# Kernel tuning notes

Measured on AMD Instinct MI355X. Metric: run time of the kernel, lower is better.

Reference implementation:

```python
import jax, jax.numpy as jnp
import numpy as np

N_NODES = 50000
N_EDGES = 1250000
D_FEAT = 64


def setup_inputs() -> dict:
    key = jax.random.key(0)
    k1, k2, k3, k4 = jax.random.split(key, 4)
    feat = jax.random.normal(k1, (N_NODES, D_FEAT), dtype=jnp.float32)
    edge_weight = jax.random.uniform(k2, (N_EDGES,), dtype=jnp.float32)
    edge_src = jax.random.randint(k3, (N_EDGES,), 0, N_NODES, dtype=jnp.int64)
    edge_dst = jnp.sort(jax.random.randint(k4, (N_EDGES,), 0, N_NODES, dtype=jnp.int64))
    return {"feat": feat, "edge_weight": edge_weight,
            "edge_src": edge_src, "edge_dst": edge_dst}


def reference(feat, edge_weight, edge_src, edge_dst):
    # u_mul_e: gather source node features, scale by per-edge weight
    msgs = feat[edge_src] * edge_weight[:, None]          # [E, d]
    # fn.sum: scatter-add messages to destination nodes
    rst = jax.ops.segment_sum(msgs, edge_dst, num_segments=N_NODES)  # [N, d]
    return rst
```

## Files before the change

kernel.cpp:

```cpp
#include <hip/hip_runtime.h>
#include <hip/hip_fp16.h>

#define D_FEAT 64

__global__ __launch_bounds__(256) void build_rowptr_scatter(
    const int* __restrict__ edge_dst, int* __restrict__ rp,
    int n_edges, int n_nodes) {
  const int e = blockIdx.x * blockDim.x + threadIdx.x;
  if (e > n_edges) return;
  const int d0 = (e == 0) ? -1 : edge_dst[e - 1];
  const int d1 = (e == n_edges) ? n_nodes : edge_dst[e];
  for (int v = d0 + 1; v <= d1; ++v) rp[v] = e;
}

__global__ __launch_bounds__(256) void repack_f16(
    const float* __restrict__ feat, uint2* __restrict__ f16,
    int n_vec4) {
  const int i = blockIdx.x * blockDim.x + threadIdx.x;
  if (i >= n_vec4) return;
  const float4 v = ((const float4*)feat)[i];
  const __half2 h0 = __float22half2_rn(make_float2(v.x, v.y));
  const __half2 h1 = __float22half2_rn(make_float2(v.z, v.w));
  uint2 o;
  o.x = *(const unsigned int*)&h0;
  o.y = *(const unsigned int*)&h1;
  f16[i] = o;
}

__global__ __launch_bounds__(256) void gcn_gather_f16(
    const uint4* __restrict__ feat16,
    const float* __restrict__ ew,
    const int* __restrict__ esrc,
    const int* __restrict__ rp,
    float* __restrict__ out, int n_nodes) {
  const int wave = (blockIdx.x * blockDim.x + threadIdx.x) >> 6;
  const int lane = threadIdx.x & 63;
  if (wave >= n_nodes) return;
  const int slot = lane >> 3;
  const int part = lane & 7;

  const int e0 = rp[wave];
  const int e1 = rp[wave + 1];

  float a0 = 0.f, a1 = 0.f, a2 = 0.f, a3 = 0.f;
  float a4 = 0.f, a5 = 0.f, a6 = 0.f, a7 = 0.f;

  for (int base = e0; base < e1; base += 64) {
    const int n = min(64, e1 - base);
    int   s = 0;
    float w = 0.0f;
    if (lane < n) {
      s = esrc[base + lane];
      w = ew[base + lane];
    }
#pragma unroll
    for (int r = 0; r < 8; ++r) {
      const int   sk = __shfl(s, r * 8 + slot);
      const float wk = __shfl(w, r * 8 + slot);
      const uint4 q  = feat16[(size_t)sk * 8 + part];
      const float2 f0 = __half22float2(*(const __half2*)&q.x);
      const float2 f1 = __half22float2(*(const __half2*)&q.y);
      const float2 f2 = __half22float2(*(const __half2*)&q.z);
      const float2 f3 = __half22float2(*(const __half2*)&q.w);
      a0 = fmaf(f0.x, wk, a0); a1 = fmaf(f0.y, wk, a1);
      a2 = fmaf(f1.x, wk, a2); a3 = fmaf(f1.y, wk, a3);
      a4 = fmaf(f2.x, wk, a4); a5 = fmaf(f2.y, wk, a5);
      a6 = fmaf(f3.x, wk, a6); a7 = fmaf(f3.y, wk, a7);
    }
  }

#pragma unroll
  for (int m = 8; m <= 32; m <<= 1) {
    a0 += __shfl_xor(a0, m); a1 += __shfl_xor(a1, m);
    a2 += __shfl_xor(a2, m); a3 += __shfl_xor(a3, m);
    a4 += __shfl_xor(a4, m); a5 += __shfl_xor(a5, m);
    a6 += __shfl_xor(a6, m); a7 += __shfl_xor(a7, m);
  }

  if (slot == 0) {
    float4* orow = (float4*)(out + (size_t)wave * D_FEAT);
    orow[part * 2]     = make_float4(a0, a1, a2, a3);
    orow[part * 2 + 1] = make_float4(a4, a5, a6, a7);
  }
}

extern "C" void kernel_launch(void* const* d_in, const int* in_sizes, int n_in,
                              void* d_out, int out_size, void* d_ws, size_t ws_size,
                              hipStream_t stream) {
  const float* feat        = (const float*)d_in[0];
  const float* edge_weight = (const float*)d_in[1];
  const int*   edge_src    = (const int*)d_in[2];
  const int*   edge_dst    = (const int*)d_in[3];
  float* out = (float*)d_out;

  const int n_edges = in_sizes[1];
  const int n_nodes = out_size / D_FEAT;

  int*  rp     = (int*)d_ws;
  uint2* f16   = (uint2*)((char*)d_ws + (1 << 20));

  const int bp_threads = n_edges + 1;
  build_rowptr_scatter<<<(bp_threads + 255) / 256, 256, 0, stream>>>(
      edge_dst, rp, n_edges, n_nodes);

  const int n_vec4 = n_nodes * (D_FEAT / 4);
  repack_f16<<<(n_vec4 + 255) / 256, 256, 0, stream>>>(feat, f16, n_vec4);

  const long total_threads = (long)n_nodes * 64;
  gcn_gather_f16<<<(int)((total_threads + 255) / 256), 256, 0, stream>>>(
      (const uint4*)f16, edge_weight, edge_src, rp, out, n_nodes);
}
```

Baseline: 105.7 us.

## Merge prep kernels into one launch and warm per-XCD caches in gather

The row-pointer build and the f16 feature repack now run in a single launch, with blocks split by index, which removes one kernel launch and its dependency gap. The gather kernel also starts with a prologue where the first blocks on each XCD (blockIdx>>3) read the whole f16 feature table, so it is resident in that XCD's L2 before the random gathers begin. The warm-up adds about 6.4 MB of reads per XCD at kernel start and assumes round-robin block-to-XCD placement.

Result: slower. 110.5 us (+4.5%).

```diff
diff --git a/kernel.cpp b/kernel.cpp
--- a/kernel.cpp
+++ b/kernel.cpp
@@ -3,28 +3,27 @@
 
 #define D_FEAT 64
 
-__global__ __launch_bounds__(256) void build_rowptr_scatter(
+__global__ __launch_bounds__(256) void prep_kernel(
+    const float* __restrict__ feat, uint2* __restrict__ f16,
     const int* __restrict__ edge_dst, int* __restrict__ rp,
-    int n_edges, int n_nodes) {
-  const int e = blockIdx.x * blockDim.x + threadIdx.x;
-  if (e > n_edges) return;
-  const int d0 = (e == 0) ? -1 : edge_dst[e - 1];
-  const int d1 = (e == n_edges) ? n_nodes : edge_dst[e];
-  for (int v = d0 + 1; v <= d1; ++v) rp[v] = e;
-}
-
-__global__ __launch_bounds__(256) void repack_f16(
-    const float* __restrict__ feat, uint2* __restrict__ f16,
-    int n_vec4) {
-  const int i = blockIdx.x * blockDim.x + threadIdx.x;
-  if (i >= n_vec4) return;
-  const float4 v = ((const float4*)feat)[i];
-  const __half2 h0 = __float22half2_rn(make_float2(v.x, v.y));
-  const __half2 h1 = __float22half2_rn(make_float2(v.z, v.w));
-  uint2 o;
-  o.x = *(const unsigned int*)&h0;
-  o.y = *(const unsigned int*)&h1;
-  f16[i] = o;
+    int n_vec4, int n_edges, int n_nodes, int rb) {
+  if ((int)blockIdx.x < rb) {
+    const int i = blockIdx.x * blockDim.x + threadIdx.x;
+    if (i >= n_vec4) return;
+    const float4 v = ((const float4*)feat)[i];
+    const __half2 h0 = __float22half2_rn(make_float2(v.x, v.y));
+    const __half2 h1 = __float22half2_rn(make_float2(v.z, v.w));
+    uint2 o;
+    o.x = *(const unsigned int*)&h0;
+    o.y = *(const unsigned int*)&h1;
+    f16[i] = o;
+  } else {
+    const int e = (blockIdx.x - rb) * blockDim.x + threadIdx.x;
+    if (e > n_edges) return;
+    const int d0 = (e == 0) ? -1 : edge_dst[e - 1];
+    const int d1 = (e == n_edges) ? n_nodes : edge_dst[e];
+    for (int v = d0 + 1; v <= d1; ++v) rp[v] = e;
+  }
 }
 
 __global__ __launch_bounds__(256) void gcn_gather_f16(
@@ -33,6 +32,21 @@
     const int* __restrict__ esrc,
     const int* __restrict__ rp,
     float* __restrict__ out, int n_nodes) {
+  const int total16 = n_nodes * 8;
+  const int warm_slices = (total16 + 1023) / 1024;
+  const int xcd_seq = blockIdx.x >> 3;
+  if (xcd_seq < warm_slices) {
+    const int s0 = xcd_seq * 1024;
+#pragma unroll
+    for (int t = 0; t < 4; ++t) {
+      const int idx = s0 + t * 256 + threadIdx.x;
+      if (idx < total16) {
+        uint4 q = feat16[idx];
+        asm volatile("" :: "v"(q.x), "v"(q.y), "v"(q.z), "v"(q.w));
+      }
+    }
+  }
+
   const int wave = (blockIdx.x * blockDim.x + threadIdx.x) >> 6;
   const int lane = threadIdx.x & 63;
   if (wave >= n_nodes) return;
@@ -96,15 +110,14 @@
   const int n_edges = in_sizes[1];
   const int n_nodes = out_size / D_FEAT;
 
-  int*  rp     = (int*)d_ws;
-  uint2* f16   = (uint2*)((char*)d_ws + (1 << 20));
-
-  const int bp_threads = n_edges + 1;
-  build_rowptr_scatter<<<(bp_threads + 255) / 256, 256, 0, stream>>>(
-      edge_dst, rp, n_edges, n_nodes);
+  int*   rp  = (int*)d_ws;
+  uint2* f16 = (uint2*)((char*)d_ws + (1 << 20));
 
   const int n_vec4 = n_nodes * (D_FEAT / 4);
-  repack_f16<<<(n_vec4 + 255) / 256, 256, 0, stream>>>(feat, f16, n_vec4);
+  const int rb = (n_vec4 + 255) / 256;
+  const int eb = (n_edges + 1 + 255) / 256;
+  prep_kernel<<<rb + eb, 256, 0, stream>>>(
+      feat, f16, edge_dst, rp, n_vec4, n_edges, n_nodes, rb);
 
   const long total_threads = (long)n_nodes * 64;
   gcn_gather_f16<<<(int)((total_threads + 255) / 256), 256, 0, stream>>>(
```
